# Kernel optimization log

Hardware: AMD Instinct MI355X
Metric: run time of the kernel (lower is better)

## Reference

```python
import jax, jax.numpy as jnp
import numpy as np

N_NODES = 100000
N_EDGES = 1600000
F_IN = 128
F_OUT = 64


def setup_inputs() -> dict:
    key = jax.random.key(0)
    k0, k1, k2, k3, k4, k5 = jax.random.split(key, 6)
    stdv = 1.0 / np.sqrt(F_OUT)
    x = jax.random.normal(k0, (N_NODES, F_IN), dtype=jnp.float32)
    edge_src = jax.random.randint(k1, (N_EDGES,), 0, N_NODES, dtype=jnp.int32)
    edge_dst = jax.random.randint(k2, (N_EDGES,), 0, N_NODES, dtype=jnp.int32)
    # normalized adjacency values (all positive, like D^-1/2 A D^-1/2 entries)
    edge_weight = jax.random.uniform(k3, (N_EDGES,), dtype=jnp.float32)
    weight = jax.random.uniform(k4, (F_IN, F_OUT), dtype=jnp.float32, minval=-stdv, maxval=stdv)
    bias = jax.random.uniform(k5, (F_OUT,), dtype=jnp.float32, minval=-stdv, maxval=stdv)
    return {"x": x, "edge_weight": edge_weight, "weight": weight, "bias": bias,
            "edge_src": edge_src, "edge_dst": edge_dst}


def reference(x, edge_weight, weight, bias, edge_src, edge_dst):
    # support = X @ W  -- dense GEMM [N, F_in] x [F_in, F_out]
    support = x @ weight
    # spmm(adj, support): adj in COO form; gather source rows, scale by edge value,
    # scatter-add into destination rows.
    msgs = support[edge_src] * edge_weight[:, None]          # [E, F_out]
    out = jax.ops.segment_sum(msgs, edge_dst, num_segments=x.shape[0])
    return out + bias
```

## Files before the change

kernel.cpp:

```cpp
#include <hip/hip_runtime.h>
#include <hip/hip_bf16.h>

#define F_IN 128
#define F_OUT 64
#define BUCKET_SHIFT 7
#define BUCKET_NODES 128
#define BUCKET_CAP 2880
#define CNT_STRIDE 16
#define NB_MAX 800
#define SCAT_CHUNK 8192
#define P1_GEMM_ROWS 128
#define LDK 136

typedef __attribute__((ext_vector_type(8))) short bf16x8;
typedef __attribute__((ext_vector_type(4))) float f32x4;

__device__ inline short bf16_bits(float f) {
  __hip_bfloat16 h = __float2bfloat16(f);
  return *reinterpret_cast<short*>(&h);
}

union Phase1Smem {
  struct { short As[P1_GEMM_ROWS][LDK]; short Bs[F_OUT][LDK]; } g;
  struct { int lhist[NB_MAX]; int lcur[NB_MAX]; int ldst[SCAT_CHUNK]; } s;
};

__global__ __launch_bounds__(512, 6) void gcn_phase1_kernel(
    const float* __restrict__ x, const float* __restrict__ w,
    __hip_bfloat16* __restrict__ support,
    const int* __restrict__ esrc, const int* __restrict__ edst,
    const float* __restrict__ ew, int* __restrict__ bcount,
    int2* __restrict__ region, int n_nodes, int n_edges, int nb,
    int n_scat_blocks) {
  __shared__ Phase1Smem sm;
  const int tid = threadIdx.x;

  if ((int)blockIdx.x < n_scat_blocks) {
    const int e0 = blockIdx.x * SCAT_CHUNK;
    const int e1 = min(e0 + SCAT_CHUNK, n_edges);
    const int n_local = e1 - e0;

    for (int i = tid; i < nb; i += 512) sm.s.lhist[i] = 0;
    __syncthreads();
    for (int i = tid; i < n_local; i += 512) {
      const int d = edst[e0 + i];
      sm.s.ldst[i] = d;
      atomicAdd(&sm.s.lhist[d >> BUCKET_SHIFT], 1);
    }
    __syncthreads();
    for (int b = tid; b < nb; b += 512) {
      const int c = sm.s.lhist[b];
      sm.s.lcur[b] = c ? atomicAdd(&bcount[b * CNT_STRIDE], c) : 0;
    }
    __syncthreads();
    for (int i = tid; i < n_local; i += 512) {
      const int d = sm.s.ldst[i];
      const int b = d >> BUCKET_SHIFT;
      const int pos = atomicAdd(&sm.s.lcur[b], 1);
      if (pos < BUCKET_CAP) {
        region[(size_t)b * BUCKET_CAP + pos] =
            make_int2((esrc[e0 + i] << BUCKET_SHIFT) | (d & (BUCKET_NODES - 1)),
                      __float_as_int(ew[e0 + i]));
      }
    }
  } else {
    const int gbid = (int)blockIdx.x - n_scat_blocks;
    const int block_row = gbid * P1_GEMM_ROWS;

#pragma unroll
    for (int i = 0; i < F_IN * F_OUT / 512; ++i) {
      const int idx = tid + i * 512;
      sm.g.Bs[idx & 63][idx >> 6] = bf16_bits(w[idx]);
    }
#pragma unroll
    for (int i = 0; i < P1_GEMM_ROWS * (F_IN / 4) / 512; ++i) {
      const int idx = tid + i * 512;
      const int row = idx >> 5;
      const int c4 = idx & 31;
      float4 v = make_float4(0.f, 0.f, 0.f, 0.f);
      if (block_row + row < n_nodes)
        v = ((const float4*)(x + (size_t)(block_row + row) * F_IN))[c4];
      short4 b;
      b.x = bf16_bits(v.x);
      b.y = bf16_bits(v.y);
      b.z = bf16_bits(v.z);
      b.w = bf16_bits(v.w);
      *(short4*)&sm.g.As[row][c4 * 4] = b;
    }
    __syncthreads();

    const int lane = tid & 63;
    const int wid = tid >> 6;
    const int wr0 = wid * 16;
    const int m = lane & 15;
    const int quad = lane >> 4;

    f32x4 acc0 = {0.f, 0.f, 0.f, 0.f};
    f32x4 acc1 = {0.f, 0.f, 0.f, 0.f};
    f32x4 acc2 = {0.f, 0.f, 0.f, 0.f};
    f32x4 acc3 = {0.f, 0.f, 0.f, 0.f};
#pragma unroll
    for (int ks = 0; ks < 4; ++ks) {
      const int ko = ks * 32 + quad * 8;
      const bf16x8 a  = *(const bf16x8*)&sm.g.As[wr0 + m][ko];
      const bf16x8 b0 = *(const bf16x8*)&sm.g.Bs[0 + m][ko];
      const bf16x8 b1 = *(const bf16x8*)&sm.g.Bs[16 + m][ko];
      const bf16x8 b2 = *(const bf16x8*)&sm.g.Bs[32 + m][ko];
      const bf16x8 b3 = *(const bf16x8*)&sm.g.Bs[48 + m][ko];
      acc0 = __builtin_amdgcn_mfma_f32_16x16x32_bf16(a, b0, acc0, 0, 0, 0);
      acc1 = __builtin_amdgcn_mfma_f32_16x16x32_bf16(a, b1, acc1, 0, 0, 0);
      acc2 = __builtin_amdgcn_mfma_f32_16x16x32_bf16(a, b2, acc2, 0, 0, 0);
      acc3 = __builtin_amdgcn_mfma_f32_16x16x32_bf16(a, b3, acc3, 0, 0, 0);
    }
#pragma unroll
    for (int r = 0; r < 4; ++r) {
      const int row = block_row + wr0 + quad * 4 + r;
      if (row < n_nodes) {
        __hip_bfloat16* op = support + (size_t)row * F_OUT;
        op[0 + m]  = __float2bfloat16(acc0[r]);
        op[16 + m] = __float2bfloat16(acc1[r]);
        op[32 + m] = __float2bfloat16(acc2[r]);
        op[48 + m] = __float2bfloat16(acc3[r]);
      }
    }
  }
}

__global__ __launch_bounds__(256) void gcn_bucket_sort_kernel(
    const int2* __restrict__ region, const int* __restrict__ bcount,
    int2* __restrict__ sorted, int* __restrict__ ends, int n_nodes, int nb) {
  __shared__ int2 eb[BUCKET_CAP];
  __shared__ int2 outb[BUCKET_CAP];
  __shared__ int lhist[BUCKET_NODES];
  __shared__ int lcur[BUCKET_NODES];
  __shared__ int redw[4];
  const int b = blockIdx.x;
  const int lane = threadIdx.x & 63;
  const int wid = threadIdx.x >> 6;

  int partial = 0;
  for (int i = threadIdx.x; i < b; i += 256) {
    const int cc = bcount[i * CNT_STRIDE];
    partial += (cc < BUCKET_CAP ? cc : BUCKET_CAP);
  }
#pragma unroll
  for (int off = 32; off >= 1; off >>= 1) partial += __shfl_xor(partial, off, 64);
  if (lane == 0) redw[wid] = partial;
  for (int i = threadIdx.x; i < BUCKET_NODES; i += 256) lhist[i] = 0;
  __syncthreads();
  const int gbase = redw[0] + redw[1] + redw[2] + redw[3];

  int cnt = bcount[b * CNT_STRIDE];
  cnt = (cnt < BUCKET_CAP ? cnt : BUCKET_CAP);
  const int node0 = b << BUCKET_SHIFT;

  for (int i = threadIdx.x; i < cnt; i += 256) {
    const int2 p = region[(size_t)b * BUCKET_CAP + i];
    eb[i] = p;
    atomicAdd(&lhist[p.x & (BUCKET_NODES - 1)], 1);
  }
  __syncthreads();
  if (threadIdx.x < 64) {
    const int v0 = lhist[lane];
    const int v1 = lhist[64 + lane];
    int s0 = v0;
#pragma unroll
    for (int off = 1; off < 64; off <<= 1) {
      const int t = __shfl_up(s0, off, 64);
      if (lane >= off) s0 += t;
    }
    const int tot0 = __shfl(s0, 63, 64);
    int s1 = v1;
#pragma unroll
    for (int off = 1; off < 64; off <<= 1) {
      const int t = __shfl_up(s1, off, 64);
      if (lane >= off) s1 += t;
    }
    s1 += tot0;
    lcur[lane] = s0 - v0;
    lcur[64 + lane] = s1 - v1;
    const int n0 = node0 + lane;
    const int n1 = node0 + 64 + lane;
    if (n0 < n_nodes) ends[n0] = gbase + s0;
    if (n1 < n_nodes) ends[n1] = gbase + s1;
  }
  __syncthreads();
  for (int i = threadIdx.x; i < cnt; i += 256) {
    const int2 p = eb[i];
    const int ldst = p.x & (BUCKET_NODES - 1);
    const int pos = atomicAdd(&lcur[ldst], 1);
    outb[pos] = make_int2(p.x >> BUCKET_SHIFT, p.y);
  }
  __syncthreads();
  for (int i = threadIdx.x; i < cnt; i += 256) {
    sorted[gbase + i] = outb[i];
  }
}

__global__ __launch_bounds__(256) void gcn_aggregate_kernel(
    const __hip_bfloat16* __restrict__ support, const int2* __restrict__ sorted,
    const int* __restrict__ ends, const float* __restrict__ bias,
    float* __restrict__ out, int n_nodes) {
  const int node = (blockIdx.x * 256 + threadIdx.x) >> 6;
  const int lane = threadIdx.x & 63;
  if (node >= n_nodes) return;
  const int r = lane >> 4;
  const int c4 = (lane & 15) * 4;
  const int start = (node == 0) ? 0 : ends[node - 1];
  const int end = ends[node];
  const ushort* sup = (const ushort*)support;

  f32x4 acc0 = {0.f, 0.f, 0.f, 0.f};
  f32x4 acc1 = {0.f, 0.f, 0.f, 0.f};
  for (int base = start; base < end; base += 64) {
    const int m = end - base;
    int2 meta = make_int2(0, 0);
    if (lane < m) meta = sorted[base + lane];
    const int m4 = (m < 64 ? m : 64);
    const int mr = (m4 + 7) & ~7;
    for (int j = 0; j < mr; j += 8) {
      const int   s0 = __shfl(meta.x, j + r, 64);
      const float w0 = __int_as_float(__shfl(meta.y, j + r, 64));
      const int   s1 = __shfl(meta.x, j + 4 + r, 64);
      const float w1 = __int_as_float(__shfl(meta.y, j + 4 + r, 64));
      const uint2 d0 = *(const uint2*)(sup + (size_t)s0 * F_OUT + c4);
      const uint2 d1 = *(const uint2*)(sup + (size_t)s1 * F_OUT + c4);
      acc0[0] = fmaf(__uint_as_float(d0.x << 16), w0, acc0[0]);
      acc0[1] = fmaf(__uint_as_float(d0.x & 0xffff0000u), w0, acc0[1]);
      acc0[2] = fmaf(__uint_as_float(d0.y << 16), w0, acc0[2]);
      acc0[3] = fmaf(__uint_as_float(d0.y & 0xffff0000u), w0, acc0[3]);
      acc1[0] = fmaf(__uint_as_float(d1.x << 16), w1, acc1[0]);
      acc1[1] = fmaf(__uint_as_float(d1.x & 0xffff0000u), w1, acc1[1]);
      acc1[2] = fmaf(__uint_as_float(d1.y << 16), w1, acc1[2]);
      acc1[3] = fmaf(__uint_as_float(d1.y & 0xffff0000u), w1, acc1[3]);
    }
  }
  f32x4 acc;
#pragma unroll
  for (int i = 0; i < 4; ++i) {
    float v = acc0[i] + acc1[i];
    v += __shfl_xor(v, 16, 64);
    v += __shfl_xor(v, 32, 64);
    acc[i] = v;
  }
  if (r == 0) {
    const float4 b4 = *(const float4*)(bias + c4);
    float4 o;
    o.x = acc[0] + b4.x;
    o.y = acc[1] + b4.y;
    o.z = acc[2] + b4.z;
    o.w = acc[3] + b4.w;
    *(float4*)(out + (size_t)node * F_OUT + c4) = o;
  }
}

extern "C" void kernel_launch(void* const* d_in, const int* in_sizes, int n_in,
                              void* d_out, int out_size, void* d_ws, size_t ws_size,
                              hipStream_t stream) {
  const float* x    = (const float*)d_in[0];
  const float* ew   = (const float*)d_in[1];
  const float* w    = (const float*)d_in[2];
  const float* bias = (const float*)d_in[3];
  const int*   esrc = (const int*)d_in[4];
  const int*   edst = (const int*)d_in[5];
  float* out = (float*)d_out;

  const int n_nodes = in_sizes[0] / F_IN;
  const int n_edges = in_sizes[4];
  const int nb = (n_nodes + BUCKET_NODES - 1) >> BUCKET_SHIFT;

  char* ws = (char*)d_ws;
  size_t off = 0;
  auto alloc = [&](size_t bytes) {
    size_t o = off;
    off += (bytes + 255) / 256 * 256;
    return o;
  };
  const size_t off_sorted  = alloc((size_t)n_edges * sizeof(int2));
  const size_t off_ends    = alloc((size_t)n_nodes * sizeof(int));
  const size_t off_bcount  = alloc((size_t)nb * CNT_STRIDE * sizeof(int));
  const size_t off_region  = alloc((size_t)nb * BUCKET_CAP * sizeof(int2));
  const size_t off_support = off;
  const size_t need_fused =
      off_support + (size_t)n_nodes * F_OUT * sizeof(__hip_bfloat16);
  const bool fused = (ws_size >= need_fused);

  int2* sorted = (int2*)(ws + off_sorted);
  int*  ends   = (int*)(ws + off_ends);
  int*  bcount = (int*)(ws + off_bcount);
  int2* region = (int2*)(ws + off_region);
  __hip_bfloat16* support =
      (__hip_bfloat16*)(ws + (fused ? off_support : off_region));

  const int scat_blocks = (n_edges + SCAT_CHUNK - 1) / SCAT_CHUNK;
  const int gemm_blocks = (n_nodes + P1_GEMM_ROWS - 1) / P1_GEMM_ROWS;

  hipMemsetAsync(bcount, 0, (size_t)nb * CNT_STRIDE * sizeof(int), stream);
  if (fused) {
    gcn_phase1_kernel<<<scat_blocks + gemm_blocks, 512, 0, stream>>>(
        x, w, support, esrc, edst, ew, bcount, region, n_nodes, n_edges, nb,
        scat_blocks);
    gcn_bucket_sort_kernel<<<nb, 256, 0, stream>>>(region, bcount, sorted,
                                                   ends, n_nodes, nb);
  } else {
    gcn_phase1_kernel<<<scat_blocks, 512, 0, stream>>>(
        x, w, support, esrc, edst, ew, bcount, region, n_nodes, n_edges, nb,
        scat_blocks);
    gcn_bucket_sort_kernel<<<nb, 256, 0, stream>>>(region, bcount, sorted,
                                                   ends, n_nodes, nb);
    gcn_phase1_kernel<<<gemm_blocks, 512, 0, stream>>>(
        x, w, support, esrc, edst, ew, bcount, region, n_nodes, n_edges, nb, 0);
  }
  gcn_aggregate_kernel<<<(int)(((size_t)n_nodes * 64 + 255) / 256), 256, 0,
                         stream>>>(support, sorted, ends, bias, out, n_nodes);
}
```

Baseline: 197.8 us.

## Fuse bucket sort with aggregation and shrink phase-1 shared memory

Merges the per-bucket sort and neighbor aggregation into one kernel, so sorted edges stay in LDS and the global sorted/ends arrays plus their write and read-back are removed. The scatter phase now re-reads edst from global memory instead of caching it in LDS. SCAT_CHUNK and GEMM tile rows change, and each GEMM wave now covers half the output columns, which raises occupancy to 8 blocks. The trade-off is that aggregation parallelism drops to about 782 blocks, each working through 16 nodes per wave serially, and the aggregation loop handles only 4 edges per step instead of 8.

```diff
diff --git a/kernel.cpp b/kernel.cpp
--- a/kernel.cpp
+++ b/kernel.cpp
@@ -8,8 +8,8 @@
 #define BUCKET_CAP 2880
 #define CNT_STRIDE 16
 #define NB_MAX 800
-#define SCAT_CHUNK 8192
-#define P1_GEMM_ROWS 128
+#define SCAT_CHUNK 16384
+#define P1_GEMM_ROWS 64
 #define LDK 136
 
 typedef __attribute__((ext_vector_type(8))) short bf16x8;
@@ -22,10 +22,10 @@
 
 union Phase1Smem {
   struct { short As[P1_GEMM_ROWS][LDK]; short Bs[F_OUT][LDK]; } g;
-  struct { int lhist[NB_MAX]; int lcur[NB_MAX]; int ldst[SCAT_CHUNK]; } s;
+  struct { int lhist[NB_MAX]; int lcur[NB_MAX]; } s;
 };
 
-__global__ __launch_bounds__(512, 6) void gcn_phase1_kernel(
+__global__ __launch_bounds__(512, 8) void gcn_phase1_kernel(
     const float* __restrict__ x, const float* __restrict__ w,
     __hip_bfloat16* __restrict__ support,
     const int* __restrict__ esrc, const int* __restrict__ edst,
@@ -43,9 +43,7 @@
     for (int i = tid; i < nb; i += 512) sm.s.lhist[i] = 0;
     __syncthreads();
     for (int i = tid; i < n_local; i += 512) {
-      const int d = edst[e0 + i];
-      sm.s.ldst[i] = d;
-      atomicAdd(&sm.s.lhist[d >> BUCKET_SHIFT], 1);
+      atomicAdd(&sm.s.lhist[edst[e0 + i] >> BUCKET_SHIFT], 1);
     }
     __syncthreads();
     for (int b = tid; b < nb; b += 512) {
@@ -54,7 +52,7 @@
     }
     __syncthreads();
     for (int i = tid; i < n_local; i += 512) {
-      const int d = sm.s.ldst[i];
+      const int d = edst[e0 + i];
       const int b = d >> BUCKET_SHIFT;
       const int pos = atomicAdd(&sm.s.lcur[b], 1);
       if (pos < BUCKET_CAP) {
@@ -91,78 +89,59 @@
 
     const int lane = tid & 63;
     const int wid = tid >> 6;
-    const int wr0 = wid * 16;
+    const int wr0 = (wid >> 1) * 16;
+    const int wc0 = (wid & 1) * 32;
     const int m = lane & 15;
     const int quad = lane >> 4;
 
     f32x4 acc0 = {0.f, 0.f, 0.f, 0.f};
     f32x4 acc1 = {0.f, 0.f, 0.f, 0.f};
-    f32x4 acc2 = {0.f, 0.f, 0.f, 0.f};
-    f32x4 acc3 = {0.f, 0.f, 0.f, 0.f};
 #pragma unroll
     for (int ks = 0; ks < 4; ++ks) {
       const int ko = ks * 32 + quad * 8;
       const bf16x8 a  = *(const bf16x8*)&sm.g.As[wr0 + m][ko];
-      const bf16x8 b0 = *(const bf16x8*)&sm.g.Bs[0 + m][ko];
-      const bf16x8 b1 = *(const bf16x8*)&sm.g.Bs[16 + m][ko];
-      const bf16x8 b2 = *(const bf16x8*)&sm.g.Bs[32 + m][ko];
-      const bf16x8 b3 = *(const bf16x8*)&sm.g.Bs[48 + m][ko];
+      const bf16x8 b0 = *(const bf16x8*)&sm.g.Bs[wc0 + m][ko];
+      const bf16x8 b1 = *(const bf16x8*)&sm.g.Bs[wc0 + 16 + m][ko];
       acc0 = __builtin_amdgcn_mfma_f32_16x16x32_bf16(a, b0, acc0, 0, 0, 0);
       acc1 = __builtin_amdgcn_mfma_f32_16x16x32_bf16(a, b1, acc1, 0, 0, 0);
-      acc2 = __builtin_amdgcn_mfma_f32_16x16x32_bf16(a, b2, acc2, 0, 0, 0);
-      acc3 = __builtin_amdgcn_mfma_f32_16x16x32_bf16(a, b3, acc3, 0, 0, 0);
     }
 #pragma unroll
     for (int r = 0; r < 4; ++r) {
       const int row = block_row + wr0 + quad * 4 + r;
       if (row < n_nodes) {
         __hip_bfloat16* op = support + (size_t)row * F_OUT;
-        op[0 + m]  = __float2bfloat16(acc0[r]);
-        op[16 + m] = __float2bfloat16(acc1[r]);
-        op[32 + m] = __float2bfloat16(acc2[r]);
-        op[48 + m] = __float2bfloat16(acc3[r]);
+        op[wc0 + m]      = __float2bfloat16(acc0[r]);
+        op[wc0 + 16 + m] = __float2bfloat16(acc1[r]);
       }
     }
   }
 }
 
-__global__ __launch_bounds__(256) void gcn_bucket_sort_kernel(
+__global__ __launch_bounds__(512, 8) void gcn_sort_agg_kernel(
+    const __hip_bfloat16* __restrict__ support,
     const int2* __restrict__ region, const int* __restrict__ bcount,
-    int2* __restrict__ sorted, int* __restrict__ ends, int n_nodes, int nb) {
-  __shared__ int2 eb[BUCKET_CAP];
+    const float* __restrict__ bias, float* __restrict__ out, int n_nodes) {
   __shared__ int2 outb[BUCKET_CAP];
-  __shared__ int lhist[BUCKET_NODES];
+  __shared__ int hist[BUCKET_NODES];
+  __shared__ int nbeg[BUCKET_NODES];
   __shared__ int lcur[BUCKET_NODES];
-  __shared__ int redw[4];
   const int b = blockIdx.x;
-  const int lane = threadIdx.x & 63;
-  const int wid = threadIdx.x >> 6;
-
-  int partial = 0;
-  for (int i = threadIdx.x; i < b; i += 256) {
-    const int cc = bcount[i * CNT_STRIDE];
-    partial += (cc < BUCKET_CAP ? cc : BUCKET_CAP);
-  }
-#pragma unroll
-  for (int off = 32; off >= 1; off >>= 1) partial += __shfl_xor(partial, off, 64);
-  if (lane == 0) redw[wid] = partial;
-  for (int i = threadIdx.x; i < BUCKET_NODES; i += 256) lhist[i] = 0;
-  __syncthreads();
-  const int gbase = redw[0] + redw[1] + redw[2] + redw[3];
+  const int tid = threadIdx.x;
+  const int lane = tid & 63;
 
   int cnt = bcount[b * CNT_STRIDE];
   cnt = (cnt < BUCKET_CAP ? cnt : BUCKET_CAP);
-  const int node0 = b << BUCKET_SHIFT;
-
-  for (int i = threadIdx.x; i < cnt; i += 256) {
-    const int2 p = region[(size_t)b * BUCKET_CAP + i];
-    eb[i] = p;
-    atomicAdd(&lhist[p.x & (BUCKET_NODES - 1)], 1);
-  }
-  __syncthreads();
-  if (threadIdx.x < 64) {
-    const int v0 = lhist[lane];
-    const int v1 = lhist[64 + lane];
+  const int2* reg = region + (size_t)b * BUCKET_CAP;
+
+  for (int i = tid; i < BUCKET_NODES; i += 512) hist[i] = 0;
+  __syncthreads();
+  for (int i = tid; i < cnt; i += 512) {
+    atomicAdd(&hist[reg[i].x & (BUCKET_NODES - 1)], 1);
+  }
+  __syncthreads();
+  if (tid < 64) {
+    const int v0 = hist[lane];
+    const int v1 = hist[64 + lane];
     int s0 = v0;
 #pragma unroll
     for (int off = 1; off < 64; off <<= 1) {
@@ -177,80 +156,56 @@
       if (lane >= off) s1 += t;
     }
     s1 += tot0;
+    nbeg[lane] = s0 - v0;
+    nbeg[64 + lane] = s1 - v1;
     lcur[lane] = s0 - v0;
     lcur[64 + lane] = s1 - v1;
-    const int n0 = node0 + lane;
-    const int n1 = node0 + 64 + lane;
-    if (n0 < n_nodes) ends[n0] = gbase + s0;
-    if (n1 < n_nodes) ends[n1] = gbase + s1;
-  }
-  __syncthreads();
-  for (int i = threadIdx.x; i < cnt; i += 256) {
-    const int2 p = eb[i];
-    const int ldst = p.x & (BUCKET_NODES - 1);
-    const int pos = atomicAdd(&lcur[ldst], 1);
+  }
+  __syncthreads();
+  for (int i = tid; i < cnt; i += 512) {
+    const int2 p = reg[i];
+    const int pos = atomicAdd(&lcur[p.x & (BUCKET_NODES - 1)], 1);
     outb[pos] = make_int2(p.x >> BUCKET_SHIFT, p.y);
   }
   __syncthreads();
-  for (int i = threadIdx.x; i < cnt; i += 256) {
-    sorted[gbase + i] = outb[i];
-  }
-}
-
-__global__ __launch_bounds__(256) void gcn_aggregate_kernel(
-    const __hip_bfloat16* __restrict__ support, const int2* __restrict__ sorted,
-    const int* __restrict__ ends, const float* __restrict__ bias,
-    float* __restrict__ out, int n_nodes) {
-  const int node = (blockIdx.x * 256 + threadIdx.x) >> 6;
-  const int lane = threadIdx.x & 63;
-  if (node >= n_nodes) return;
+
+  const int wid = tid >> 6;
   const int r = lane >> 4;
   const int c4 = (lane & 15) * 4;
-  const int start = (node == 0) ? 0 : ends[node - 1];
-  const int end = ends[node];
   const ushort* sup = (const ushort*)support;
-
-  f32x4 acc0 = {0.f, 0.f, 0.f, 0.f};
-  f32x4 acc1 = {0.f, 0.f, 0.f, 0.f};
-  for (int base = start; base < end; base += 64) {
-    const int m = end - base;
-    int2 meta = make_int2(0, 0);
-    if (lane < m) meta = sorted[base + lane];
-    const int m4 = (m < 64 ? m : 64);
-    const int mr = (m4 + 7) & ~7;
-    for (int j = 0; j < mr; j += 8) {
-      const int   s0 = __shfl(meta.x, j + r, 64);
-      const float w0 = __int_as_float(__shfl(meta.y, j + r, 64));
-      const int   s1 = __shfl(meta.x, j + 4 + r, 64);
-      const float w1 = __int_as_float(__shfl(meta.y, j + 4 + r, 64));
-      const uint2 d0 = *(const uint2*)(sup + (size_t)s0 * F_OUT + c4);
-      const uint2 d1 = *(const uint2*)(sup + (size_t)s1 * F_OUT + c4);
-      acc0[0] = fmaf(__uint_as_float(d0.x << 16), w0, acc0[0]);
-      acc0[1] = fmaf(__uint_as_float(d0.x & 0xffff0000u), w0, acc0[1]);
-      acc0[2] = fmaf(__uint_as_float(d0.y << 16), w0, acc0[2]);
-      acc0[3] = fmaf(__uint_as_float(d0.y & 0xffff0000u), w0, acc0[3]);
-      acc1[0] = fmaf(__uint_as_float(d1.x << 16), w1, acc1[0]);
-      acc1[1] = fmaf(__uint_as_float(d1.x & 0xffff0000u), w1, acc1[1]);
-      acc1[2] = fmaf(__uint_as_float(d1.y << 16), w1, acc1[2]);
-      acc1[3] = fmaf(__uint_as_float(d1.y & 0xffff0000u), w1, acc1[3]);
-    }
-  }
-  f32x4 acc;
-#pragma unroll
-  for (int i = 0; i < 4; ++i) {
-    float v = acc0[i] + acc1[i];
-    v += __shfl_xor(v, 16, 64);
-    v += __shfl_xor(v, 32, 64);
-    acc[i] = v;
-  }
-  if (r == 0) {
-    const float4 b4 = *(const float4*)(bias + c4);
-    float4 o;
-    o.x = acc[0] + b4.x;
-    o.y = acc[1] + b4.y;
-    o.z = acc[2] + b4.z;
-    o.w = acc[3] + b4.w;
-    *(float4*)(out + (size_t)node * F_OUT + c4) = o;
+  const float4 b4 = *(const float4*)(bias + c4);
+  for (int nl = wid * 16; nl < wid * 16 + 16; ++nl) {
+    const int g = (b << BUCKET_SHIFT) + nl;
+    if (g >= n_nodes) break;
+    const int s = nbeg[nl];
+    const int e = lcur[nl];
+    f32x4 acc = {0.f, 0.f, 0.f, 0.f};
+    for (int j = s; j < e; j += 4) {
+      const int jr = j + r;
+      const bool valid = jr < e;
+      const int2 meta = outb[valid ? jr : e - 1];
+      const float wv = valid ? __int_as_float(meta.y) : 0.f;
+      const uint2 d = *(const uint2*)(sup + (size_t)meta.x * F_OUT + c4);
+      acc[0] = fmaf(__uint_as_float(d.x << 16), wv, acc[0]);
+      acc[1] = fmaf(__uint_as_float(d.x & 0xffff0000u), wv, acc[1]);
+      acc[2] = fmaf(__uint_as_float(d.y << 16), wv, acc[2]);
+      acc[3] = fmaf(__uint_as_float(d.y & 0xffff0000u), wv, acc[3]);
+    }
+#pragma unroll
+    for (int i = 0; i < 4; ++i) {
+      float v = acc[i];
+      v += __shfl_xor(v, 16, 64);
+      v += __shfl_xor(v, 32, 64);
+      acc[i] = v;
+    }
+    if (r == 0) {
+      float4 o;
+      o.x = acc[0] + b4.x;
+      o.y = acc[1] + b4.y;
+      o.z = acc[2] + b4.z;
+      o.w = acc[3] + b4.w;
+      *(float4*)(out + (size_t)g * F_OUT + c4) = o;
+    }
   }
 }
 
@@ -276,41 +231,22 @@
     off += (bytes + 255) / 256 * 256;
     return o;
   };
-  const size_t off_sorted  = alloc((size_t)n_edges * sizeof(int2));
-  const size_t off_ends    = alloc((size_t)n_nodes * sizeof(int));
   const size_t off_bcount  = alloc((size_t)nb * CNT_STRIDE * sizeof(int));
   const size_t off_region  = alloc((size_t)nb * BUCKET_CAP * sizeof(int2));
-  const size_t off_support = off;
-  const size_t need_fused =
-      off_support + (size_t)n_nodes * F_OUT * sizeof(__hip_bfloat16);
-  const bool fused = (ws_size >= need_fused);
-
-  int2* sorted = (int2*)(ws + off_sorted);
-  int*  ends   = (int*)(ws + off_ends);
+  const size_t off_support = alloc((size_t)n_nodes * F_OUT * sizeof(__hip_bfloat16));
+  (void)off_support;
+
   int*  bcount = (int*)(ws + off_bcount);
   int2* region = (int2*)(ws + off_region);
-  __hip_bfloat16* support =
-      (__hip_bfloat16*)(ws + (fused ? off_support : off_region));
+  __hip_bfloat16* support = (__hip_bfloat16*)(ws + off_support);
 
   const int scat_blocks = (n_edges + SCAT_CHUNK - 1) / SCAT_CHUNK;
   const int gemm_blocks = (n_nodes + P1_GEMM_ROWS - 1) / P1_GEMM_ROWS;
 
   hipMemsetAsync(bcount, 0, (size_t)nb * CNT_STRIDE * sizeof(int), stream);
-  if (fused) {
-    gcn_phase1_kernel<<<scat_blocks + gemm_blocks, 512, 0, stream>>>(
-        x, w, support, esrc, edst, ew, bcount, region, n_nodes, n_edges, nb,
-        scat_blocks);
-    gcn_bucket_sort_kernel<<<nb, 256, 0, stream>>>(region, bcount, sorted,
-                                                   ends, n_nodes, nb);
-  } else {
-    gcn_phase1_kernel<<<scat_blocks, 512, 0, stream>>>(
-        x, w, support, esrc, edst, ew, bcount, region, n_nodes, n_edges, nb,
-        scat_blocks);
-    gcn_bucket_sort_kernel<<<nb, 256, 0, stream>>>(region, bcount, sorted,
-                                                   ends, n_nodes, nb);
-    gcn_phase1_kernel<<<gemm_blocks, 512, 0, stream>>>(
-        x, w, support, esrc, edst, ew, bcount, region, n_nodes, n_edges, nb, 0);
-  }
-  gcn_aggregate_kernel<<<(int)(((size_t)n_nodes * 64 + 255) / 256), 256, 0,
-                         stream>>>(support, sorted, ends, bias, out, n_nodes);
-}
+  gcn_phase1_kernel<<<scat_blocks + gemm_blocks, 512, 0, stream>>>(
+      x, w, support, esrc, edst, ew, bcount, region, n_nodes, n_edges, nb,
+      scat_blocks);
+  gcn_sort_agg_kernel<<<nb, 512, 0, stream>>>(support, region, bcount, bias,
+                                              out, n_nodes);
+}
```

After: 197.3 us. Within noise of the previous version (-0.2%).
